# Optimization experiments

Hardware: AMD Instinct MI355X
Metric: run time of the kernel (lower is better)

Reference implementation:

```python
import jax, jax.numpy as jnp
import numpy as np

MASK_VALUE = 0.0

def setup_inputs() -> dict:
    key = jax.random.key(0)
    k1, k2, k3 = jax.random.split(key, 3)
    B, N, F, K = 8, 10000, 64, 8
    inp = jax.random.normal(k1, (B, N, F), dtype=jnp.float32)
    inds = jax.random.randint(k2, (B, N, K), 0, N, dtype=jnp.int32)
    # sprinkle some negative (masked) indices, like padded neighbor slots
    neg = jax.random.uniform(k3, (B, N, K)) < 0.1
    inds = jnp.where(neg, jnp.int32(-1), inds)
    return {"inp": inp, "inds": inds}

def reference(inp, inds):
    B, N, F = inp.shape
    K = inds.shape[-1]
    inp_p = inp.reshape(-1, F)                      # [B*N, F]
    inds_p = inds.reshape(-1, K)                    # [B*N, K]
    # which sequence each flat row belongs to, offset into flat node table
    seq_offset = (jnp.arange(inds_p.shape[0], dtype=jnp.int32) // N) * N
    mask = inds_p >= 0
    # wrap local index by N (faithful to tf.mod), add per-sequence offset
    offset = jnp.where(mask, (inds_p % N) + seq_offset[:, None],
                       jnp.int32(B * N))            # masked -> sentinel row
    # append mask-value row so sentinel index gathers mask_value features
    table = jnp.concatenate(
        [inp_p, jnp.full((1, F), MASK_VALUE, dtype=inp.dtype)], axis=0)
    neighb = table[offset]                          # [B*N, K, F] gather
    neighb = neighb.reshape(B, N, K, F)
    # include_self: concat self features as extra neighbor slot
    out = jnp.concatenate([neighb, inp[:, :, None, :]], axis=2)  # [B,N,K+1,F]
    return out
```

## Files before the change

kernel.cpp:

```cpp
#include <hip/hip_runtime.h>


typedef float f32x4 __attribute__((ext_vector_type(4)));

constexpr int B    = 8;
constexpr int N    = 10000;
constexpr int F    = 64;
constexpr int K    = 8;
constexpr int KP1  = K + 1;
constexpr int ROWS_PER_BATCH  = N * KP1;
constexpr int ROWS_PER_BLOCK  = 16;
constexpr int BLOCKS_PER_BATCH = ROWS_PER_BATCH / ROWS_PER_BLOCK;
constexpr int NBLOCKS = BLOCKS_PER_BATCH * B;

__global__ __launch_bounds__(256)
void GatherFromIndices_kernel(const float* __restrict__ inp,
                              const int*   __restrict__ inds,
                              float*       __restrict__ out) {
    int b     = blockIdx.x & 7;
    int chunk = blockIdx.x >> 3;
    int t     = threadIdx.x;
    int lr    = t >> 4;
    int lane  = t & 15;

    int row_in_batch = chunk * ROWS_PER_BLOCK + lr;
    int n  = row_in_batch / KP1;
    int k  = row_in_batch - n * KP1;
    int bn = b * N + n;

    f32x4 v;
    if (k == K) {
        v = ((const f32x4*)(inp + (size_t)bn * F))[lane];
    } else {
        int idx = inds[bn * K + k];
        if (idx < 0) {
            v = (f32x4){0.f, 0.f, 0.f, 0.f};
        } else {
            int row = b * N + (idx % N);
            v = ((const f32x4*)(inp + (size_t)row * F))[lane];
        }
    }
    size_t r = (size_t)b * ROWS_PER_BATCH + row_in_batch;
    __builtin_nontemporal_store(v, ((f32x4*)out) + r * 16 + lane);
}

extern "C" void kernel_launch(void* const* d_in, const int* in_sizes, int n_in,
                              void* d_out, int out_size, void* d_ws, size_t ws_size,
                              hipStream_t stream) {
    const float* inp  = (const float*)d_in[0];
    const int*   inds = (const int*)d_in[1];
    float*       out  = (float*)d_out;

    GatherFromIndices_kernel<<<NBLOCKS, 256, 0, stream>>>(inp, inds, out);
}
```

Baseline: 224.9 us.

## Process all batches per thread with batched loads and branchless gather

```diff
diff --git a/kernel.cpp b/kernel.cpp
--- a/kernel.cpp
+++ b/kernel.cpp
@@ -8,40 +8,45 @@
 constexpr int F    = 64;
 constexpr int K    = 8;
 constexpr int KP1  = K + 1;
-constexpr int ROWS_PER_BATCH  = N * KP1;
-constexpr int ROWS_PER_BLOCK  = 16;
-constexpr int BLOCKS_PER_BATCH = ROWS_PER_BATCH / ROWS_PER_BLOCK;
-constexpr int NBLOCKS = BLOCKS_PER_BATCH * B;
+constexpr int ROWS_PER_BATCH = N * KP1;
+constexpr int NTHREADS = ROWS_PER_BATCH * 16;
+constexpr int NBLOCKS  = NTHREADS / 256;
 
 __global__ __launch_bounds__(256)
 void GatherFromIndices_kernel(const float* __restrict__ inp,
                               const int*   __restrict__ inds,
                               float*       __restrict__ out) {
-    int b     = blockIdx.x & 7;
-    int chunk = blockIdx.x >> 3;
-    int t     = threadIdx.x;
-    int lr    = t >> 4;
-    int lane  = t & 15;
+    int t    = blockIdx.x * 256 + threadIdx.x;
+    int rg   = t >> 4;
+    int lane = t & 15;
 
-    int row_in_batch = chunk * ROWS_PER_BLOCK + lr;
-    int n  = row_in_batch / KP1;
-    int k  = row_in_batch - n * KP1;
-    int bn = b * N + n;
+    int n  = rg / KP1;
+    int kk = rg - n * KP1;
+    bool self  = (kk == K);
+    int  kload = self ? 0 : kk;
 
-    f32x4 v;
-    if (k == K) {
-        v = ((const f32x4*)(inp + (size_t)bn * F))[lane];
-    } else {
-        int idx = inds[bn * K + k];
-        if (idx < 0) {
-            v = (f32x4){0.f, 0.f, 0.f, 0.f};
-        } else {
-            int row = b * N + (idx % N);
-            v = ((const f32x4*)(inp + (size_t)row * F))[lane];
-        }
+    int idx[B];
+#pragma unroll
+    for (int b = 0; b < B; ++b) {
+        int iv = inds[(b * N + n) * K + kload];
+        idx[b] = self ? n : iv;
     }
-    size_t r = (size_t)b * ROWS_PER_BATCH + row_in_batch;
-    __builtin_nontemporal_store(v, ((f32x4*)out) + r * 16 + lane);
+
+    f32x4 v[B];
+#pragma unroll
+    for (int b = 0; b < B; ++b) {
+        int  iv  = idx[b];
+        int  m   = iv % N;
+        int  row = (iv < 0) ? 0 : (b * N + m);
+        f32x4 ld = ((const f32x4*)(inp + (size_t)row * F))[lane];
+        v[b] = (iv < 0) ? (f32x4)(0.f) : ld;
+    }
+
+#pragma unroll
+    for (int b = 0; b < B; ++b) {
+        size_t r = (size_t)b * ROWS_PER_BATCH + rg;
+        ((f32x4*)out)[r * 16 + lane] = v[b];
+    }
 }
 
 extern "C" void kernel_launch(void* const* d_in, const int* in_sizes, int n_in,
```

New measurement: 209.5 us. -6.8%, faster.
